# Performance work log

Measured on AMD Instinct MI355X. Metric: run time of the kernel, lower is better.

Reference implementation:

```python
import jax, jax.numpy as jnp
import numpy as np

N = 1024   # num nodes (assets)
F = 128    # node feature dim (node_dim)
M = 256    # memory_dim (scorer hidden)
E = 8      # edge_dim
BN_EPS = 1e-5


def setup_inputs() -> dict:
    key = jax.random.key(0)
    ks = jax.random.split(key, 6)
    x = jax.random.normal(ks[0], (N, F), dtype=jnp.float32)
    ctx = jax.random.uniform(ks[1], (4,), dtype=jnp.float32)  # [crisis_prob, ttc/30, urgency, confidence]
    W1 = jax.random.normal(ks[2], (M, 2 * F + 4), dtype=jnp.float32) * 0.05
    b1 = jnp.zeros((M,), jnp.float32)
    gamma = jnp.ones((M,), jnp.float32)
    beta = jnp.zeros((M,), jnp.float32)
    run_mean = jnp.zeros((M,), jnp.float32)
    run_var = jnp.ones((M,), jnp.float32)
    W2 = jax.random.normal(ks[3], (E, M), dtype=jnp.float32) * 0.05
    b2 = jnp.zeros((E,), jnp.float32)
    W3 = jax.random.normal(ks[4], (1, E), dtype=jnp.float32) * 0.05
    b3 = jnp.zeros((1,), jnp.float32)
    return {"x": x, "ctx": ctx, "W1": W1, "b1": b1, "gamma": gamma, "beta": beta,
            "run_mean": run_mean, "run_var": run_var, "W2": W2, "b2": b2, "W3": W3, "b3": b3}


def reference(x, ctx, W1, b1, gamma, beta, run_mean, run_var, W2, b2, W3, b3):
    # All unordered pairs i<j (static shapes); original loops over stressed pairs only,
    # we score all pairs and expose the stressed/threshold filter as a boolean mask.
    ii, jj = jnp.triu_indices(N, k=1)  # each [P], P = N*(N-1)/2

    # First linear decomposed: W1 @ [x_i; x_j; ctx] = A x_i + B x_j + (C ctx + b1)
    pa = x @ W1[:, :F].T          # [N, M]
    pb = x @ W1[:, F:2 * F].T     # [N, M]
    cterm = ctx @ W1[:, 2 * F:].T + b1  # [M]

    h = jax.nn.relu(pa[ii] + pb[jj] + cterm)                           # [P, M]
    h = gamma * (h - run_mean) * jax.lax.rsqrt(run_var + BN_EPS) + beta  # eval-mode BatchNorm1d
    h = jax.nn.relu(h @ W2.T + b2)                                     # [P, E]
    scores = jax.nn.sigmoid(h @ W3.T + b3)[:, 0]                       # [P]

    # Stressed-node selection: std over feature dim > mean std (torch unbiased std)
    stress = x.std(axis=1, ddof=1)
    stressed = stress > stress.mean()
    edge_mask = (scores > 0.5) & stressed[ii] & stressed[jj]           # [P] bool
    return scores, edge_mask
```

## Files before the change

kernel.cpp:

```cpp
#include <hip/hip_runtime.h>
#include <math.h>

#define N_NODES 1024
#define F_DIM   128
#define M_DIM   256
#define E_DIM   8
#define P_PAIRS 523776
#define NBLK    1056
#define APITCH  33

typedef float v2f __attribute__((ext_vector_type(2)));

__global__ __launch_bounds__(256) void kA(const float* __restrict__ x,
                                          const float* __restrict__ ctx,
                                          const float* __restrict__ W1,
                                          const float* __restrict__ b1,
                                          const float* __restrict__ gamma,
                                          const float* __restrict__ beta,
                                          const float* __restrict__ rmean,
                                          const float* __restrict__ rvar,
                                          const float* __restrict__ W2,
                                          const float* __restrict__ b2,
                                          float* __restrict__ pa,
                                          float* __restrict__ pb,
                                          float* __restrict__ stress,
                                          float* __restrict__ w2ft,
                                          float* __restrict__ b2f) {
  const int t = threadIdx.x;

  if (blockIdx.x == 256) {
    __shared__ float bnbs[256];
    const float s   = gamma[t] / sqrtf(rvar[t] + 1e-5f);
    bnbs[t] = beta[t] - s * rmean[t];
    #pragma unroll
    for (int e = 0; e < 8; ++e) w2ft[t * 8 + e] = W2[e * 256 + t] * s;
    __syncthreads();
    const int wv = t >> 6, lane = t & 63;
    #pragma unroll
    for (int r = 0; r < 2; ++r) {
      const int e = wv * 2 + r;
      float acc = 0.f;
      #pragma unroll
      for (int k = 0; k < 4; ++k) acc += W2[e * 256 + lane + 64 * k] * bnbs[lane + 64 * k];
      #pragma unroll
      for (int m = 32; m > 0; m >>= 1) acc += __shfl_xor(acc, m, 64);
      if (lane == 0) b2f[e] = acc + b2[e];
    }
    return;
  }

  __shared__ float xv[4][128];
  const int n0 = blockIdx.x * 4;
  if (t < 128) {
    ((float4*)&xv[0][0])[t] = ((const float4*)(x + (size_t)n0 * F_DIM))[t];
  }
  __syncthreads();

  {
    const int wv = t >> 6, lane = t & 63;
    const float a = xv[wv][lane], b = xv[wv][lane + 64];
    float sum = a + b;
    #pragma unroll
    for (int m = 32; m > 0; m >>= 1) sum += __shfl_xor(sum, m, 64);
    const float mean = sum * (1.0f / 128.0f);
    const float d0 = a - mean, d1 = b - mean;
    float ss = d0 * d0 + d1 * d1;
    #pragma unroll
    for (int m = 32; m > 0; m >>= 1) ss += __shfl_xor(ss, m, 64);
    if (lane == 0) stress[n0 + wv] = sqrtf(ss * (1.0f / 127.0f));
  }

  const float4* wrow = (const float4*)(W1 + (size_t)t * 260);
  float accA[4] = {0.f, 0.f, 0.f, 0.f};
  float accB[4] = {0.f, 0.f, 0.f, 0.f};
  #pragma unroll 8
  for (int k4 = 0; k4 < 32; ++k4) {
    const float4 wa = wrow[k4];
    const float4 wb = wrow[32 + k4];
    #pragma unroll
    for (int nn = 0; nn < 4; ++nn) {
      const float4 xf = ((const float4*)&xv[nn][0])[k4];
      accA[nn] = fmaf(xf.w, wa.w, fmaf(xf.z, wa.z, fmaf(xf.y, wa.y, fmaf(xf.x, wa.x, accA[nn]))));
      accB[nn] = fmaf(xf.w, wb.w, fmaf(xf.z, wb.z, fmaf(xf.y, wb.y, fmaf(xf.x, wb.x, accB[nn]))));
    }
  }
  const float c0 = ctx[0], c1 = ctx[1], c2 = ctx[2], c3 = ctx[3];
  const float* rowt = W1 + (size_t)t * 260 + 256;
  const float ctv = b1[t] + c0 * rowt[0] + c1 * rowt[1] + c2 * rowt[2] + c3 * rowt[3];
  #pragma unroll
  for (int nn = 0; nn < 4; ++nn) {
    pa[(size_t)(n0 + nn) * M_DIM + t] = accA[nn] + ctv;
    pb[(size_t)(n0 + nn) * M_DIM + t] = accB[nn];
  }
}

__global__ __launch_bounds__(256, 6) void kC(const float* __restrict__ pa,
                                             const float* __restrict__ pb,
                                             const float* __restrict__ w2ft,
                                             const float* __restrict__ b2f,
                                             const float* __restrict__ W3,
                                             const float* __restrict__ b3,
                                             const float* __restrict__ stress,
                                             float* __restrict__ out) {
  __shared__ float4 a4[16 * APITCH];
  __shared__ float4 b4[32 * APITCH];
  const int t = threadIdx.x;

  const int p = blockIdx.x;
  int tj = (int)((sqrtf(4.0f * (float)p + 1.0f) - 1.0f) * 0.5f);
  while ((tj + 1) * (tj + 2) <= p) ++tj;
  while (tj * (tj + 1) > p) --tj;
  const int si = p - tj * (tj + 1);
  const int i0 = si * 16, j0 = tj * 32;

  const float4* pa4 = (const float4*)pa;
  const float4* pb4 = (const float4*)pb;
  const double* wdp = (const double*)w2ft;

  float4 rA[2], rB[4];
  #pragma unroll
  for (int q = 0; q < 2; ++q) {
    const int d = q * 256 + t, r = d >> 5, c = d & 31;
    rA[q] = pa4[(size_t)(i0 + r) * 64 + c];
  }
  #pragma unroll
  for (int q = 0; q < 4; ++q) {
    const int d = q * 256 + t, r = d >> 5, c = d & 31;
    rB[q] = pb4[(size_t)(j0 + r) * 64 + c];
  }

  float ssum = 0.f;
  {
    const int lane = t & 63;
    #pragma unroll
    for (int k = 0; k < 16; ++k) ssum += stress[lane + 64 * k];
    #pragma unroll
    for (int m = 32; m > 0; m >>= 1) ssum += __shfl_xor(ssum, m, 64);
  }
  const float smean = ssum * (1.0f / 1024.0f);

  #pragma unroll
  for (int q = 0; q < 2; ++q) {
    const int d = q * 256 + t, r = d >> 5, c = d & 31;
    a4[r * APITCH + c] = rA[q];
  }
  #pragma unroll
  for (int q = 0; q < 4; ++q) {
    const int d = q * 256 + t, r = d >> 5, c = d & 31;
    b4[r * APITCH + c] = rB[q];
  }
  __syncthreads();

  const int jx = t & 15;
  const int iy = t >> 4;
  v2f acc[8];
  #pragma unroll
  for (int e = 0; e < 8; ++e) acc[e] = (v2f){0.f, 0.f};

  const float4* aRow  = a4 + iy * APITCH;
  const float4* bRow0 = b4 + jx * APITCH;
  const float4* bRow1 = b4 + (jx + 16) * APITCH;

  auto computeChunk = [&](int cw) {
    #pragma unroll 2
    for (int m4 = 0; m4 < 32; ++m4) {
      const float4 A  = aRow[m4];
      const float4 B0 = bRow0[m4];
      const float4 B1 = bRow1[m4];
      const double* wr = wdp + (size_t)(cw + m4) * 16;
      const float* Af  = (const float*)&A;
      const float* B0f = (const float*)&B0;
      const float* B1f = (const float*)&B1;
      #pragma unroll
      for (int mm = 0; mm < 4; ++mm) {
        v2f R;
        R.x = fmaxf(Af[mm] + B0f[mm], 0.f);
        R.y = fmaxf(Af[mm] + B1f[mm], 0.f);
        #pragma unroll
        for (int k = 0; k < 4; ++k) {
          const double wp = wr[mm * 4 + k];
          asm("v_pk_fma_f32 %0, %1, %2, %0 op_sel:[0,0,0] op_sel_hi:[0,1,1]"
              : "+v"(acc[2 * k]) : "s"(wp), "v"(R));
          asm("v_pk_fma_f32 %0, %1, %2, %0 op_sel:[1,0,0] op_sel_hi:[1,1,1]"
              : "+v"(acc[2 * k + 1]) : "s"(wp), "v"(R));
        }
      }
    }
  };

  computeChunk(0);
  __syncthreads();

  #pragma unroll
  for (int q = 0; q < 2; ++q) {
    const int d = q * 256 + t, r = d >> 5, c = d & 31;
    rA[q] = pa4[(size_t)(i0 + r) * 64 + 32 + c];
  }
  #pragma unroll
  for (int q = 0; q < 4; ++q) {
    const int d = q * 256 + t, r = d >> 5, c = d & 31;
    rB[q] = pb4[(size_t)(j0 + r) * 64 + 32 + c];
  }
  #pragma unroll
  for (int q = 0; q < 2; ++q) {
    const int d = q * 256 + t, r = d >> 5, c = d & 31;
    a4[r * APITCH + c] = rA[q];
  }
  #pragma unroll
  for (int q = 0; q < 4; ++q) {
    const int d = q * 256 + t, r = d >> 5, c = d & 31;
    b4[r * APITCH + c] = rB[q];
  }
  __syncthreads();

  computeChunk(32);

  float w3v[8], b2v[8];
  #pragma unroll
  for (int e = 0; e < 8; ++e) { w3v[e] = W3[e]; b2v[e] = b2f[e]; }
  const float b3v = b3[0];
  const int i = i0 + iy;
  #pragma unroll
  for (int jb = 0; jb < 2; ++jb) {
    const int j = j0 + jx + jb * 16;
    if (i < j) {
      float logit = b3v;
      #pragma unroll
      for (int e = 0; e < 8; ++e) {
        const float av = jb ? acc[e].y : acc[e].x;
        const float h2 = fmaxf(av + b2v[e], 0.f);
        logit = fmaf(w3v[e], h2, logit);
      }
      const float score = 1.0f / (1.0f + expf(-logit));
      const int idx = i * 1023 - (i * (i - 1)) / 2 + (j - i - 1);
      out[idx] = score;
      const bool mk = (score > 0.5f) && (stress[i] > smean) && (stress[j] > smean);
      out[P_PAIRS + idx] = mk ? 1.0f : 0.0f;
    }
  }
}

extern "C" void kernel_launch(void* const* d_in, const int* in_sizes, int n_in,
                              void* d_out, int out_size, void* d_ws, size_t ws_size,
                              hipStream_t stream) {
  const float* x     = (const float*)d_in[0];
  const float* ctx   = (const float*)d_in[1];
  const float* W1    = (const float*)d_in[2];
  const float* b1    = (const float*)d_in[3];
  const float* gamma = (const float*)d_in[4];
  const float* beta  = (const float*)d_in[5];
  const float* rmean = (const float*)d_in[6];
  const float* rvar  = (const float*)d_in[7];
  const float* W2    = (const float*)d_in[8];
  const float* b2    = (const float*)d_in[9];
  const float* W3    = (const float*)d_in[10];
  const float* b3    = (const float*)d_in[11];
  float* out = (float*)d_out;

  float* ws     = (float*)d_ws;
  float* pa     = ws;
  float* pb     = pa + 262144;
  float* w2ft   = pb + 262144;
  float* b2f    = w2ft + 2048;
  float* stress = b2f + 8;

  hipLaunchKernelGGL(kA, dim3(257), dim3(256), 0, stream, x, ctx, W1, b1, gamma, beta,
                     rmean, rvar, W2, b2, pa, pb, stress, w2ft, b2f);
  hipLaunchKernelGGL(kC, dim3(NBLK), dim3(256), 0, stream, pa, pb, w2ft, b2f,
                     W3, b3, stress, out);
}
```

Measured before the change: 120.1 us.

## Stage W1 through padded LDS chunks and process eight nodes per kA block

The projection kernel kA now handles 8 nodes per block instead of 4 and launches 129 blocks instead of 257. It stages W1 through a padded shared-memory tile in 32-column chunks, using coalesced loads and a barrier per chunk, in place of strided per-thread global row reads. The aim is to cut uncoalesced W1 traffic and reuse each weight across more nodes. The inner loop reads x from global memory rather than from the shared xv copy, which relies on the cache and may add load pressure. The change also halves the number of blocks, which lowers parallelism in a kernel that is small next to kC.

New measurement: 131.1 us. 9.2% more time.

```diff
diff --git a/kernel.cpp b/kernel.cpp
--- a/kernel.cpp
+++ b/kernel.cpp
@@ -8,6 +8,7 @@
 #define P_PAIRS 523776
 #define NBLK    1056
 #define APITCH  33
+#define WPITCH  36
 
 typedef float v2f __attribute__((ext_vector_type(2)));
 
@@ -28,7 +29,7 @@
                                           float* __restrict__ b2f) {
   const int t = threadIdx.x;
 
-  if (blockIdx.x == 256) {
+  if (blockIdx.x == 128) {
     __shared__ float bnbs[256];
     const float s   = gamma[t] / sqrtf(rvar[t] + 1e-5f);
     bnbs[t] = beta[t] - s * rmean[t];
@@ -49,46 +50,82 @@
     return;
   }
 
-  __shared__ float xv[4][128];
-  const int n0 = blockIdx.x * 4;
-  if (t < 128) {
-    ((float4*)&xv[0][0])[t] = ((const float4*)(x + (size_t)n0 * F_DIM))[t];
+  __shared__ float wt[256 * WPITCH];
+  __shared__ float xv[8][128];
+  const int n0 = blockIdx.x * 8;
+
+  {
+    const int row = t >> 5, c4 = t & 31;
+    *(float4*)&xv[row][c4 * 4] = ((const float4*)(x + (size_t)(n0 + row) * F_DIM))[c4];
+  }
+  {
+    const int r = t >> 3, c4 = t & 7;
+    #pragma unroll
+    for (int q = 0; q < 8; ++q) {
+      const int rr = q * 32 + r;
+      *(float4*)&wt[rr * WPITCH + c4 * 4] =
+          ((const float4*)W1)[(size_t)rr * 65 + c4];
+    }
   }
   __syncthreads();
 
   {
     const int wv = t >> 6, lane = t & 63;
-    const float a = xv[wv][lane], b = xv[wv][lane + 64];
-    float sum = a + b;
-    #pragma unroll
-    for (int m = 32; m > 0; m >>= 1) sum += __shfl_xor(sum, m, 64);
-    const float mean = sum * (1.0f / 128.0f);
-    const float d0 = a - mean, d1 = b - mean;
-    float ss = d0 * d0 + d1 * d1;
-    #pragma unroll
-    for (int m = 32; m > 0; m >>= 1) ss += __shfl_xor(ss, m, 64);
-    if (lane == 0) stress[n0 + wv] = sqrtf(ss * (1.0f / 127.0f));
-  }
-
-  const float4* wrow = (const float4*)(W1 + (size_t)t * 260);
-  float accA[4] = {0.f, 0.f, 0.f, 0.f};
-  float accB[4] = {0.f, 0.f, 0.f, 0.f};
-  #pragma unroll 8
-  for (int k4 = 0; k4 < 32; ++k4) {
-    const float4 wa = wrow[k4];
-    const float4 wb = wrow[32 + k4];
-    #pragma unroll
-    for (int nn = 0; nn < 4; ++nn) {
-      const float4 xf = ((const float4*)&xv[nn][0])[k4];
-      accA[nn] = fmaf(xf.w, wa.w, fmaf(xf.z, wa.z, fmaf(xf.y, wa.y, fmaf(xf.x, wa.x, accA[nn]))));
-      accB[nn] = fmaf(xf.w, wb.w, fmaf(xf.z, wb.z, fmaf(xf.y, wb.y, fmaf(xf.x, wb.x, accB[nn]))));
-    }
-  }
+    #pragma unroll
+    for (int s2 = 0; s2 < 2; ++s2) {
+      const int n = wv * 2 + s2;
+      const float a = xv[n][lane], b = xv[n][lane + 64];
+      float sum = a + b;
+      #pragma unroll
+      for (int m = 32; m > 0; m >>= 1) sum += __shfl_xor(sum, m, 64);
+      const float mean = sum * (1.0f / 128.0f);
+      const float d0 = a - mean, d1 = b - mean;
+      float ss = d0 * d0 + d1 * d1;
+      #pragma unroll
+      for (int m = 32; m > 0; m >>= 1) ss += __shfl_xor(ss, m, 64);
+      if (lane == 0) stress[n0 + n] = sqrtf(ss * (1.0f / 127.0f));
+    }
+  }
+
+  float accA[8] = {0.f,0.f,0.f,0.f,0.f,0.f,0.f,0.f};
+  float accB[8] = {0.f,0.f,0.f,0.f,0.f,0.f,0.f,0.f};
+
+  for (int c = 0; c < 8; ++c) {
+    {
+      const int kbase = (c & 3) * 32;
+      float4 wreg[8];
+      #pragma unroll
+      for (int k4 = 0; k4 < 8; ++k4) wreg[k4] = *(const float4*)&wt[t * WPITCH + k4 * 4];
+      float* acc = (c < 4) ? accA : accB;
+      #pragma unroll
+      for (int k4 = 0; k4 < 8; ++k4) {
+        const float4 w4 = wreg[k4];
+        #pragma unroll
+        for (int nn = 0; nn < 8; ++nn) {
+          const float* xr = x + (size_t)(n0 + nn) * F_DIM + kbase + k4 * 4;
+          acc[nn] = fmaf(xr[3], w4.w, fmaf(xr[2], w4.z, fmaf(xr[1], w4.y, fmaf(xr[0], w4.x, acc[nn]))));
+        }
+      }
+    }
+    if (c < 7) {
+      __syncthreads();
+      const int r = t >> 3, c4 = t & 7;
+      const int coff4 = (c + 1 < 4) ? (c + 1) * 8 : 32 + (c + 1 - 4) * 8;
+      #pragma unroll
+      for (int q = 0; q < 8; ++q) {
+        const int rr = q * 32 + r;
+        *(float4*)&wt[rr * WPITCH + c4 * 4] =
+            ((const float4*)W1)[(size_t)rr * 65 + coff4 + c4];
+      }
+      __syncthreads();
+    }
+  }
+
   const float c0 = ctx[0], c1 = ctx[1], c2 = ctx[2], c3 = ctx[3];
   const float* rowt = W1 + (size_t)t * 260 + 256;
   const float ctv = b1[t] + c0 * rowt[0] + c1 * rowt[1] + c2 * rowt[2] + c3 * rowt[3];
   #pragma unroll
-  for (int nn = 0; nn < 4; ++nn) {
+  for (int nn = 0; nn < 8; ++nn) {
     pa[(size_t)(n0 + nn) * M_DIM + t] = accA[nn] + ctv;
     pb[(size_t)(n0 + nn) * M_DIM + t] = accB[nn];
   }
@@ -264,7 +301,7 @@
   float* b2f    = w2ft + 2048;
   float* stress = b2f + 8;
 
-  hipLaunchKernelGGL(kA, dim3(257), dim3(256), 0, stream, x, ctx, W1, b1, gamma, beta,
+  hipLaunchKernelGGL(kA, dim3(129), dim3(256), 0, stream, x, ctx, W1, b1, gamma, beta,
                      rmean, rvar, W2, b2, pa, pb, stress, w2ft, b2f);
   hipLaunchKernelGGL(kC, dim3(NBLK), dim3(256), 0, stream, pa, pb, w2ft, b2f,
                      W3, b3, stress, out);
```
